# Kernel optimization log

Hardware: AMD Instinct MI355X
Metric: run time of the kernel (lower is better)

The kernel has to match this reference:

```python
import jax, jax.numpy as jnp
import numpy as np

B, R, H, W = 128, 8, 256, 256


def _conv(x, w, b):
    # x: [1, C_in, h, w], w: [C_out, C_in, 3, 3]; stride 2, pad 1, then bias + ReLU
    y = jax.lax.conv_general_dilated(
        x, w, window_strides=(2, 2), padding=((1, 1), (1, 1)),
        dimension_numbers=('NCHW', 'OIHW', 'NCHW'))
    return jax.nn.relu(y + b[None, :, None, None])


def _single(x, w1, b1, w2, b2, w3, b3, fw, fb):
    # x: [3, H, W]; one sample through its region's CNN expert
    h = x[None]                      # [1,3,H,W]
    h = _conv(h, w1, b1)             # [1,32,H/2,W/2]
    h = _conv(h, w2, b2)             # [1,64,H/4,W/4]
    h = _conv(h, w3, b3)             # [1,128,H/8,W/8]
    feat = h.mean(axis=(2, 3))[0]    # [128] global average pool
    return fw @ feat + fb            # [num_classes]


def setup_inputs() -> dict:
    key = jax.random.key(0)
    ks = jax.random.split(key, 10)
    s = 0.05
    return {
        'image': jax.random.normal(ks[0], (B, 3, H, W), jnp.float32),
        'region': jax.random.randint(ks[1], (B,), 0, R, jnp.int64),
        'w1': jax.random.normal(ks[2], (R, 32, 3, 3, 3), jnp.float32) * s,
        'b1': jax.random.normal(ks[3], (R, 32), jnp.float32) * s,
        'w2': jax.random.normal(ks[4], (R, 64, 32, 3, 3), jnp.float32) * s,
        'b2': jax.random.normal(ks[5], (R, 64), jnp.float32) * s,
        'w3': jax.random.normal(ks[6], (R, 128, 64, 3, 3), jnp.float32) * s,
        'b3': jax.random.normal(ks[7], (R, 128), jnp.float32) * s,
        'fw': jax.random.normal(ks[8], (R, 2, 128), jnp.float32) * s,
        'fb': jax.random.normal(ks[9], (R, 2), jnp.float32) * s,
    }


def reference(image, region, w1, b1, w2, b2, w3, b3, fw, fb):
    # MoE-style dispatch: gather each sample's region weights, vmap per-sample expert.
    r = region.astype(jnp.int32)
    pw = [jnp.take(p, r, axis=0) for p in (w1, b1, w2, b2, w3, b3, fw, fb)]
    out = jax.vmap(_single)(image, *pw)  # [B, num_classes]
    return out
```

## Files before the change

### kernel.cpp

```cpp
#include <hip/hip_runtime.h>
#include <cstdint>


typedef __attribute__((ext_vector_type(8))) short short8;
typedef __attribute__((ext_vector_type(4))) float floatx4;
typedef __attribute__((ext_vector_type(4))) unsigned short ushort4v;
typedef __attribute__((ext_vector_type(4))) float float4v;

__device__ inline unsigned short f2bf(float f) {
  union { float f; unsigned u; } x;
  x.f = f;
  unsigned u = x.u;
  u += 0x7FFFu + ((u >> 16) & 1u);
  return (unsigned short)(u >> 16);
}

__device__ inline void g2l16(const unsigned short* g, unsigned short* l) {
  __builtin_amdgcn_global_load_lds(
      (const __attribute__((address_space(1))) unsigned int*)g,
      (__attribute__((address_space(3))) unsigned int*)(unsigned int)(uintptr_t)l,
      16, 0, 0);
}

__global__ __launch_bounds__(256) void setup_k(
    const int* __restrict__ rp, int* __restrict__ rout, float* __restrict__ feat,
    const float* __restrict__ w1, unsigned short* __restrict__ w1p,
    const float* __restrict__ w2, unsigned short* __restrict__ w2p,
    const float* __restrict__ w3, unsigned short* __restrict__ w3p,
    unsigned short* __restrict__ h2p, int nhalo) {
  const int tid = threadIdx.x;
  if (blockIdx.x == 0) {
    __shared__ int is64;
    if (tid == 0) {
      int odd_or = 0;
      for (int i = 0; i < 64; ++i) odd_or |= rp[2 * i + 1];
      is64 = (odd_or == 0) ? 1 : 0;
    }
    __syncthreads();
    if (tid < 128) {
      int r = is64 ? rp[2 * tid] : rp[tid];
      rout[tid] = r & 7;
      float* fr = feat + tid * 128;
      for (int j = 0; j < 128; ++j) fr[j] = 0.f;
    }
    return;
  }
  int t = (blockIdx.x - 1) * 256 + tid;
  if (t < 16384) {
    int j = t & 7, lane = (t >> 3) & 63, mt = (t >> 9) & 1, kg = (t >> 10) & 1,
        r = t >> 11;
    int oc = mt * 16 + (lane & 15);
    int q = (lane >> 4) & 3;
    int row = kg * 2 + (q >> 1);
    int idx = (q & 1) * 8 + j;
    int kx = idx >> 2, c = idx & 3;
    float val = 0.f;
    if (row < 3 && kx < 3 && c < 3)
      val = w1[((r * 32 + oc) * 3 + c) * 9 + row * 3 + kx];
    w1p[t] = f2bf(val);
  } else if (t < 163840) {
    int t2 = t - 16384;
    int j = t2 & 7, lane = (t2 >> 3) & 63;
    int u = t2 >> 9;
    int mt = u & 3; u >>= 2;
    int tap = u % 9;
    int r = u / 9;
    int oc = mt * 16 + (lane & 15);
    int ic = ((lane >> 4) & 3) * 8 + j;
    w2p[t2] = f2bf(w2[((r * 64 + oc) * 32 + ic) * 9 + tap]);
  } else if (t < 753664) {
    int t3 = t - 163840;
    int j = t3 & 7, lane = (t3 >> 3) & 63;
    int u = t3 >> 9;
    int mt = u & 7; u >>= 3;
    int s = u & 1; u >>= 1;
    int tap = u % 9;
    int r = u / 9;
    int oc = mt * 16 + (lane & 15);
    int ic = s * 32 + ((lane >> 4) & 3) * 8 + j;
    w3p[t3] = f2bf(w3[((r * 128 + oc) * 64 + ic) * 9 + tap]);
  } else {
    int th = t - 753664;
    if (th < nhalo) {
      int s = th / 260, i = th - s * 260;
      int y, x;
      if (i < 66) { y = 0; x = i; }
      else if (i < 132) { y = 65; x = i - 66; }
      else {
        int ii = i - 132;
        y = 1 + (ii >> 1);
        x = (ii & 1) ? 65 : 0;
      }
      short8 z = {0, 0, 0, 0, 0, 0, 0, 0};
      *(short8*)(h2p + ((size_t)s * 66 * 66 + y * 66 + x) * 8) = z;
    }
  }
}

__global__ __launch_bounds__(256, 3) void conv12_k(
    const float* __restrict__ img, const unsigned short* __restrict__ w1p,
    const float* __restrict__ b1, const unsigned short* __restrict__ w2p,
    const float* __restrict__ b2, const int* __restrict__ rgn,
    unsigned short* __restrict__ outp, int b0) {
  __shared__ unsigned short imgT[11 * 168 * 4];
  __shared__ unsigned short h1T[9 * 4 * 66 * 8];
  __shared__ float sB1[32];
  __shared__ float sB2[64];
  const int tid = threadIdx.x;
  const int xh = blockIdx.x;
  const int oy0 = blockIdx.y * 4;
  const int bl = blockIdx.z;
  const int r = __builtin_amdgcn_readfirstlane(rgn[b0 + bl]);
  if (tid < 32) sB1[tid] = b1[r * 32 + tid];
  if (tid >= 64 && tid < 128) sB2[tid - 64] = b2[r * 64 + (tid - 64)];
  const float* ib = img + (size_t)(b0 + bl) * 3 * 65536;
  const int padx = xh ? 65 : 0;
  const bool skiptop = (oy0 == 0);
  const int rb = xh * 128 - 4;

  const int n = tid & 15, q = (tid >> 4) & 3, wv = tid >> 6;
  const int lane = tid & 63;
  const short8* wpb1 = (const short8*)w1p + (size_t)r * 256 + lane;
  short8 afr1[2][2];
#pragma unroll
  for (int kg = 0; kg < 2; ++kg)
#pragma unroll
    for (int m = 0; m < 2; ++m) afr1[kg][m] = wpb1[(kg * 2 + m) * 64];

  {
    const int nch = 11 * 41;
    for (int seg = 0; seg < nch; seg += 256) {
      int c = seg + tid;
      if (c < nch) {
        int i = c / 41, cq = c - i * 41;
        int rv = 4 * oy0 - 3 + i;
        int cb = rb + 4 * cq;
        unsigned short* dp = &imgT[((size_t)i * 168 + (4 * cq - 1)) * 4];
        if (rv >= 0 && cq > 0 && cb >= 0 && cb + 3 <= 255) {
          const float* p = ib + (size_t)rv * 256 + cb;
          float4v a = *(const float4v*)p;
          float4v bb = *(const float4v*)(p + 65536);
          float4v cc = *(const float4v*)(p + 131072);
#pragma unroll
          for (int e = 0; e < 4; ++e) {
            ushort4v v = {f2bf(a[e]), f2bf(bb[e]), f2bf(cc[e]), 0};
            *(ushort4v*)(dp + e * 4) = v;
          }
        } else {
          for (int e = (cq == 0 ? 1 : 0); e < 4; ++e) {
            int cc2 = cb + e;
            ushort4v v = {0, 0, 0, 0};
            if (rv >= 0 && cc2 >= 0 && cc2 <= 255) {
              const float* p = ib + (size_t)rv * 256 + cc2;
              v.x = f2bf(p[0]);
              v.y = f2bf(p[65536]);
              v.z = f2bf(p[131072]);
            }
            *(ushort4v*)(dp + e * 4) = v;
          }
        }
      }
    }
  }
  {
    short8 z8 = {0, 0, 0, 0, 0, 0, 0, 0};
    if (tid < 36) {
      int hy = tid / 4, cg = tid % 4;
      *(short8*)&h1T[(((size_t)hy * 4 + cg) * 66 + padx) * 8] = z8;
    }
    if (skiptop) {
      for (int c = tid; c < 264; c += 256) {
        int cg = c / 66, x = c - cg * 66;
        *(short8*)&h1T[(((size_t)0 * 4 + cg) * 66 + x) * 8] = z8;
      }
    }
  }

  auto CONV1ROW = [&](int hy, int phaseB) {
    floatx4 a1[5][2];
#pragma unroll
    for (int nt = 0; nt < 5; ++nt)
#pragma unroll
      for (int m = 0; m < 2; ++m) a1[nt][m] = (floatx4){0.f, 0.f, 0.f, 0.f};
#pragma unroll
    for (int kg = 0; kg < 2; ++kg) {
      int row = kg * 2 + (q >> 1);
      int rowc = (row < 3) ? row : 0;
      int tr = 2 * hy + rowc;
      int slot = phaseB ? (tr >= 11 ? tr - 11 : tr) : tr;
#pragma unroll
      for (int nt = 0; nt < 5; ++nt) {
        int lx = nt * 16 + n;
        short8 bfr = *(const short8*)&imgT[((size_t)slot * 168 + 2 * lx) * 4 +
                                           (q & 1) * 8];
#pragma unroll
        for (int m = 0; m < 2; ++m)
          a1[nt][m] = __builtin_amdgcn_mfma_f32_16x16x32_bf16(
              afr1[kg][m], bfr, a1[nt][m], 0, 0, 0);
      }
    }
#pragma unroll
    for (int nt = 0; nt < 5; ++nt) {
      int lx = nt * 16 + n;
      bool ok = (lx <= 65) && (lx != padx) && !(skiptop && hy == 0);
      if (ok) {
#pragma unroll
        for (int m = 0; m < 2; ++m) {
          ushort4v st;
#pragma unroll
          for (int rr = 0; rr < 4; ++rr) {
            float v = a1[nt][m][rr] + sB1[m * 16 + q * 4 + rr];
            st[rr] = f2bf(v > 0.f ? v : 0.f);
          }
          int cg = m * 2 + (q >> 1);
          *(ushort4v*)&h1T[(((size_t)hy * 4 + cg) * 66 + lx) * 8 +
                           (q & 1) * 4] = st;
        }
      }
    }
  };

  __syncthreads();

  float4v Lb0[3], Lb1[3];
  int ok0 = 0, ok1 = 0;
  {
    int c = tid;
    int i = c / 41, cq = c - i * 41;
    int cb = rb + 4 * cq;
    if (cq > 0 && cb >= 0 && cb + 3 <= 255) {
      const float* p = ib + (size_t)(4 * oy0 + 8 + i) * 256 + cb;
      Lb0[0] = *(const float4v*)p;
      Lb0[1] = *(const float4v*)(p + 65536);
      Lb0[2] = *(const float4v*)(p + 131072);
      ok0 = 1;
    }
    c = tid + 256;
    if (c < 328) {
      i = c / 41; cq = c - i * 41; cb = rb + 4 * cq;
      if (cq > 0 && cb >= 0 && cb + 3 <= 255) {
        const float* p = ib + (size_t)(4 * oy0 + 8 + i) * 256 + cb;
        Lb1[0] = *(const float4v*)p;
        Lb1[1] = *(const float4v*)(p + 65536);
        Lb1[2] = *(const float4v*)(p + 131072);
        ok1 = 1;
      }
    }
  }

  for (int hy = wv; hy <= 4; hy += 4) CONV1ROW(hy, 0);
  __syncthreads();

  auto STOREB = [&](int c, const float4v* L, int okf) {
    int i = c / 41, cq = c - i * 41;
    int cb = rb + 4 * cq;
    unsigned short* dp = &imgT[((size_t)i * 168 + (4 * cq - 1)) * 4];
    if (okf) {
#pragma unroll
      for (int e = 0; e < 4; ++e) {
        ushort4v v = {f2bf(L[0][e]), f2bf(L[1][e]), f2bf(L[2][e]), 0};
        *(ushort4v*)(dp + e * 4) = v;
      }
    } else {
      int rv = 4 * oy0 + 8 + i;
      for (int e = (cq == 0 ? 1 : 0); e < 4; ++e) {
        int cc2 = cb + e;
        ushort4v v = {0, 0, 0, 0};
        if (cc2 >= 0 && cc2 <= 255) {
          const float* p = ib + (size_t)rv * 256 + cc2;
          v.x = f2bf(p[0]);
          v.y = f2bf(p[65536]);
          v.z = f2bf(p[131072]);
        }
        *(ushort4v*)(dp + e * 4) = v;
      }
    }
  };
  STOREB(tid, Lb0, ok0);
  if (tid + 256 < 328) STOREB(tid + 256, Lb1, ok1);
  __syncthreads();

  CONV1ROW(5 + wv, 1);
  __syncthreads();

  const short8* wpb2 = (const short8*)w2p + (size_t)r * 9 * 4 * 64 + lane;
  floatx4 a2[2][4];
#pragma unroll
  for (int nt = 0; nt < 2; ++nt)
#pragma unroll
    for (int m = 0; m < 4; ++m) a2[nt][m] = (floatx4){0.f, 0.f, 0.f, 0.f};
#pragma unroll
  for (int tap = 0; tap < 9; ++tap) {
    const int ky = tap / 3, kx = tap % 3;
    short8 af[4];
#pragma unroll
    for (int m = 0; m < 4; ++m) af[m] = wpb2[(tap * 4 + m) * 64];
    short8 bf[2];
#pragma unroll
    for (int nt = 0; nt < 2; ++nt) {
      int ox = nt * 16 + n;
      bf[nt] = *(const short8*)&h1T[((((2 * wv + ky) << 2) + q) * 66 +
                                    (2 * ox + kx)) * 8];
    }
#pragma unroll
    for (int m = 0; m < 4; ++m)
#pragma unroll
      for (int nt = 0; nt < 2; ++nt)
        a2[nt][m] = __builtin_amdgcn_mfma_f32_16x16x32_bf16(af[m], bf[nt],
                                                            a2[nt][m], 0, 0, 0);
  }
  unsigned short* ob = outp + (size_t)bl * 8 * 66 * 66 * 8;
  const int oy = oy0 + wv;
#pragma unroll
  for (int nt = 0; nt < 2; ++nt) {
    int ox = xh * 32 + nt * 16 + n;
#pragma unroll
    for (int m = 0; m < 4; ++m) {
      ushort4v st;
#pragma unroll
      for (int rr = 0; rr < 4; ++rr) {
        float v = a2[nt][m][rr] + sB2[m * 16 + q * 4 + rr];
        st[rr] = f2bf(v > 0.f ? v : 0.f);
      }
      int cg = m * 2 + (q >> 1);
      *(ushort4v*)&ob[(((size_t)cg * 66 + oy + 1) * 66 + ox + 1) * 8 +
                      (q & 1) * 4] = st;
    }
  }
}

__global__ __launch_bounds__(256, 3) void conv3dir_k(
    const unsigned short* __restrict__ in, const unsigned short* __restrict__ wp,
    const float* __restrict__ bias, const int* __restrict__ rgn,
    float* __restrict__ feat, int b0) {
  __shared__ float sBias[128];
  __shared__ float sGap[4 * 128];
  const int tid = threadIdx.x;
  const int bl = blockIdx.y;
  const int b = b0 + bl;
  const int r = __builtin_amdgcn_readfirstlane(rgn[b]);
  if (tid < 128) sBias[tid] = bias[r * 128 + tid];
  const int oy0 = blockIdx.x * 4;
  const unsigned short* gbase = in + (size_t)bl * 8 * 66 * 66 * 8;
  const int lane = tid & 63, wv = tid >> 6;
  const int n = lane & 15, q = (lane >> 4) & 3;
  const short8* wpb = (const short8*)wp + (size_t)r * 9 * 2 * 8 * 64 + lane;

  floatx4 acc[2][8];
#pragma unroll
  for (int nt = 0; nt < 2; ++nt)
#pragma unroll
    for (int m = 0; m < 8; ++m) acc[nt][m] = (floatx4){0.f, 0.f, 0.f, 0.f};

#pragma unroll
  for (int s = 0; s < 2; ++s) {
    const unsigned short* ab = gbase + (size_t)(s * 4 + q) * 66 * 66 * 8;
#pragma unroll
    for (int tap = 0; tap < 9; ++tap) {
      const int ky = tap / 3, kx = tap % 3;
      short8 bfr[2];
#pragma unroll
      for (int nt = 0; nt < 2; ++nt) {
        int ox = nt * 16 + n;
        bfr[nt] = *(const short8*)&ab[((size_t)(2 * oy0 + 2 * wv + ky) * 66 +
                                       (2 * ox + kx)) * 8];
      }
      short8 afr[8];
#pragma unroll
      for (int m = 0; m < 8; ++m) afr[m] = wpb[((tap * 2 + s) * 8 + m) * 64];
#pragma unroll
      for (int m = 0; m < 8; ++m)
#pragma unroll
        for (int nt = 0; nt < 2; ++nt)
          acc[nt][m] = __builtin_amdgcn_mfma_f32_16x16x32_bf16(afr[m], bfr[nt],
                                                               acc[nt][m], 0, 0, 0);
    }
  }

#pragma unroll
  for (int m = 0; m < 8; ++m)
#pragma unroll
    for (int rr = 0; rr < 4; ++rr) {
      float bv = sBias[m * 16 + q * 4 + rr];
      float vs = 0.f;
#pragma unroll
      for (int nt = 0; nt < 2; ++nt) {
        float v = acc[nt][m][rr] + bv;
        vs += (v > 0.f ? v : 0.f);
      }
      vs += __shfl_xor(vs, 1, 16);
      vs += __shfl_xor(vs, 2, 16);
      vs += __shfl_xor(vs, 4, 16);
      vs += __shfl_xor(vs, 8, 16);
      if (n == 0) sGap[wv * 128 + m * 16 + q * 4 + rr] = vs;
    }
  __syncthreads();
  if (tid < 128)
    atomicAdd(&feat[b * 128 + tid],
              sGap[tid] + sGap[128 + tid] + sGap[256 + tid] + sGap[384 + tid]);
}

__global__ __launch_bounds__(256) void head_k(
    const float* __restrict__ feat, const float* __restrict__ fw,
    const float* __restrict__ fb, const int* __restrict__ rgn,
    float* __restrict__ out) {
  int t = threadIdx.x;
  int b = t >> 1, c = t & 1;
  int r = rgn[b];
  const float* fwr = fw + (r * 2 + c) * 128;
  const float* fv = feat + b * 128;
  float a = 0.f;
#pragma unroll 8
  for (int j = 0; j < 128; ++j) a = fmaf(fwr[j], fv[j], a);
  out[t] = a * (1.0f / 1024.0f) + fb[r * 2 + c];
}

extern "C" void kernel_launch(void* const* d_in, const int* in_sizes, int n_in,
                              void* d_out, int out_size, void* d_ws, size_t ws_size,
                              hipStream_t stream) {
  const float* img = (const float*)d_in[0];
  const int* rgn_raw = (const int*)d_in[1];
  const float* w1 = (const float*)d_in[2];
  const float* b1 = (const float*)d_in[3];
  const float* w2 = (const float*)d_in[4];
  const float* b2 = (const float*)d_in[5];
  const float* w3 = (const float*)d_in[6];
  const float* b3 = (const float*)d_in[7];
  const float* fw = (const float*)d_in[8];
  const float* fb = (const float*)d_in[9];
  float* out = (float*)d_out;

  const size_t h2p_s = (size_t)8 * 66 * 66 * 8 * 2;
  const size_t per_sample = h2p_s;
  const size_t fixed = (size_t)16384 * 2 + (size_t)147456 * 2 +
                       (size_t)589824 * 2 + 128 * 128 * 4 + 512 + 16 * 256;
  int C = 128;
  while (C > 1 && fixed + (size_t)C * per_sample > ws_size) C >>= 1;

  char* ws = (char*)d_ws;
  size_t off = 0;
  auto alloc = [&](size_t bytes) {
    char* p = ws + off;
    off += (bytes + 255) & ~(size_t)255;
    return p;
  };
  unsigned short* h2p = (unsigned short*)alloc((size_t)C * h2p_s);
  unsigned short* w1p = (unsigned short*)alloc((size_t)16384 * 2);
  unsigned short* w2p = (unsigned short*)alloc((size_t)147456 * 2);
  unsigned short* w3p = (unsigned short*)alloc((size_t)589824 * 2);
  float* feat = (float*)alloc((size_t)128 * 128 * 4);
  int* rgn = (int*)alloc((size_t)128 * 4);

  {
    int nhalo = C * 8 * 260;
    int total = 753664 + nhalo;
    int nblk = 1 + (total + 255) / 256;
    hipLaunchKernelGGL(setup_k, dim3(nblk), dim3(256), 0, stream,
                       rgn_raw, rgn, feat, w1, w1p, w2, w2p, w3, w3p, h2p, nhalo);
  }

  for (int b0 = 0; b0 < 128; b0 += C) {
    hipLaunchKernelGGL(conv12_k, dim3(2, 16, C), dim3(256), 0, stream,
                       img, w1p, b1, w2p, b2, rgn, h2p, b0);
    hipLaunchKernelGGL(conv3dir_k, dim3(8, C), dim3(256), 0, stream,
                       h2p, w3p, b3, rgn, feat, b0);
  }
  hipLaunchKernelGGL(head_k, dim3(1), dim3(256), 0, stream, feat, fw, fb, rgn, out);
}
```

Baseline: 293.6 us.

## Double output rows per conv3 block, launch conv3 once over full batch

The conv3 kernel now computes two output rows per wave, so each block covers eight rows and half as many blocks are launched. Each loaded weight fragment is reused across twice as many MFMAs, at the cost of more accumulator registers (occupancy hint lowered from 3 to 2). The workspace chunking logic is removed in favour of a fixed full-batch buffer: conv12 runs in two 64-sample launches and conv3 runs once over all 128 samples. The setup kernel's region-dtype check also changes from a serial loop to a wavefront ballot. Dropping the workspace-size check risks overflowing a smaller workspace.

Result: no change. 291.1 us (-0.8%).

```diff
diff --git a/kernel.cpp b/kernel.cpp
--- a/kernel.cpp
+++ b/kernel.cpp
@@ -31,10 +31,10 @@
   const int tid = threadIdx.x;
   if (blockIdx.x == 0) {
     __shared__ int is64;
-    if (tid == 0) {
-      int odd_or = 0;
-      for (int i = 0; i < 64; ++i) odd_or |= rp[2 * i + 1];
-      is64 = (odd_or == 0) ? 1 : 0;
+    if (tid < 64) {
+      int v = rp[2 * tid + 1];
+      unsigned long long ball = __ballot(v != 0);
+      if (tid == 0) is64 = (ball == 0ULL) ? 1 : 0;
     }
     __syncthreads();
     if (tid < 128) {
@@ -329,7 +329,7 @@
   }
 }
 
-__global__ __launch_bounds__(256, 3) void conv3dir_k(
+__global__ __launch_bounds__(256, 2) void conv3dir2_k(
     const unsigned short* __restrict__ in, const unsigned short* __restrict__ wp,
     const float* __restrict__ bias, const int* __restrict__ rgn,
     float* __restrict__ feat, int b0) {
@@ -340,17 +340,19 @@
   const int b = b0 + bl;
   const int r = __builtin_amdgcn_readfirstlane(rgn[b]);
   if (tid < 128) sBias[tid] = bias[r * 128 + tid];
-  const int oy0 = blockIdx.x * 4;
+  const int oyb = blockIdx.x * 8;
   const unsigned short* gbase = in + (size_t)bl * 8 * 66 * 66 * 8;
   const int lane = tid & 63, wv = tid >> 6;
   const int n = lane & 15, q = (lane >> 4) & 3;
   const short8* wpb = (const short8*)wp + (size_t)r * 9 * 2 * 8 * 64 + lane;
 
-  floatx4 acc[2][8];
-#pragma unroll
-  for (int nt = 0; nt < 2; ++nt)
-#pragma unroll
-    for (int m = 0; m < 8; ++m) acc[nt][m] = (floatx4){0.f, 0.f, 0.f, 0.f};
+  floatx4 acc[2][2][8];
+#pragma unroll
+  for (int r2 = 0; r2 < 2; ++r2)
+#pragma unroll
+    for (int nt = 0; nt < 2; ++nt)
+#pragma unroll
+      for (int m = 0; m < 8; ++m) acc[r2][nt][m] = (floatx4){0.f, 0.f, 0.f, 0.f};
 
 #pragma unroll
   for (int s = 0; s < 2; ++s) {
@@ -358,22 +360,27 @@
 #pragma unroll
     for (int tap = 0; tap < 9; ++tap) {
       const int ky = tap / 3, kx = tap % 3;
-      short8 bfr[2];
-#pragma unroll
-      for (int nt = 0; nt < 2; ++nt) {
-        int ox = nt * 16 + n;
-        bfr[nt] = *(const short8*)&ab[((size_t)(2 * oy0 + 2 * wv + ky) * 66 +
-                                       (2 * ox + kx)) * 8];
-      }
+      short8 bfr[2][2];
+#pragma unroll
+      for (int r2 = 0; r2 < 2; ++r2)
+#pragma unroll
+        for (int nt = 0; nt < 2; ++nt) {
+          int oy = oyb + 2 * wv + r2;
+          int ox = nt * 16 + n;
+          bfr[r2][nt] = *(const short8*)&ab[((size_t)(2 * oy + ky) * 66 +
+                                             (2 * ox + kx)) * 8];
+        }
       short8 afr[8];
 #pragma unroll
       for (int m = 0; m < 8; ++m) afr[m] = wpb[((tap * 2 + s) * 8 + m) * 64];
 #pragma unroll
       for (int m = 0; m < 8; ++m)
 #pragma unroll
-        for (int nt = 0; nt < 2; ++nt)
-          acc[nt][m] = __builtin_amdgcn_mfma_f32_16x16x32_bf16(afr[m], bfr[nt],
-                                                               acc[nt][m], 0, 0, 0);
+        for (int r2 = 0; r2 < 2; ++r2)
+#pragma unroll
+          for (int nt = 0; nt < 2; ++nt)
+            acc[r2][nt][m] = __builtin_amdgcn_mfma_f32_16x16x32_bf16(
+                afr[m], bfr[r2][nt], acc[r2][nt][m], 0, 0, 0);
     }
   }
 
@@ -384,10 +391,12 @@
       float bv = sBias[m * 16 + q * 4 + rr];
       float vs = 0.f;
 #pragma unroll
-      for (int nt = 0; nt < 2; ++nt) {
-        float v = acc[nt][m][rr] + bv;
-        vs += (v > 0.f ? v : 0.f);
-      }
+      for (int r2 = 0; r2 < 2; ++r2)
+#pragma unroll
+        for (int nt = 0; nt < 2; ++nt) {
+          float v = acc[r2][nt][m][rr] + bv;
+          vs += (v > 0.f ? v : 0.f);
+        }
       vs += __shfl_xor(vs, 1, 16);
       vs += __shfl_xor(vs, 2, 16);
       vs += __shfl_xor(vs, 4, 16);
@@ -431,11 +440,6 @@
   float* out = (float*)d_out;
 
   const size_t h2p_s = (size_t)8 * 66 * 66 * 8 * 2;
-  const size_t per_sample = h2p_s;
-  const size_t fixed = (size_t)16384 * 2 + (size_t)147456 * 2 +
-                       (size_t)589824 * 2 + 128 * 128 * 4 + 512 + 16 * 256;
-  int C = 128;
-  while (C > 1 && fixed + (size_t)C * per_sample > ws_size) C >>= 1;
 
   char* ws = (char*)d_ws;
   size_t off = 0;
@@ -444,7 +448,7 @@
     off += (bytes + 255) & ~(size_t)255;
     return p;
   };
-  unsigned short* h2p = (unsigned short*)alloc((size_t)C * h2p_s);
+  unsigned short* h2p = (unsigned short*)alloc((size_t)128 * h2p_s);
   unsigned short* w1p = (unsigned short*)alloc((size_t)16384 * 2);
   unsigned short* w2p = (unsigned short*)alloc((size_t)147456 * 2);
   unsigned short* w3p = (unsigned short*)alloc((size_t)589824 * 2);
@@ -452,18 +456,19 @@
   int* rgn = (int*)alloc((size_t)128 * 4);
 
   {
-    int nhalo = C * 8 * 260;
+    int nhalo = 128 * 8 * 260;
     int total = 753664 + nhalo;
     int nblk = 1 + (total + 255) / 256;
     hipLaunchKernelGGL(setup_k, dim3(nblk), dim3(256), 0, stream,
                        rgn_raw, rgn, feat, w1, w1p, w2, w2p, w3, w3p, h2p, nhalo);
   }
 
-  for (int b0 = 0; b0 < 128; b0 += C) {
-    hipLaunchKernelGGL(conv12_k, dim3(2, 16, C), dim3(256), 0, stream,
-                       img, w1p, b1, w2p, b2, rgn, h2p, b0);
-    hipLaunchKernelGGL(conv3dir_k, dim3(8, C), dim3(256), 0, stream,
-                       h2p, w3p, b3, rgn, feat, b0);
-  }
+  for (int b0 = 0; b0 < 128; b0 += 64) {
+    hipLaunchKernelGGL(conv12_k, dim3(2, 16, 64), dim3(256), 0, stream,
+                       img, w1p, b1, w2p, b2, rgn,
+                       h2p + (size_t)b0 * 8 * 66 * 66 * 8, b0);
+  }
+  hipLaunchKernelGGL(conv3dir2_k, dim3(4, 128), dim3(256), 0, stream,
+                     h2p, w3p, b3, rgn, feat, 0);
   hipLaunchKernelGGL(head_k, dim3(1), dim3(256), 0, stream, feat, fw, fb, rgn, out);
 }
```
